# Optimization experiments

Hardware: AMD Instinct MI355X
Metric: run time of the kernel (lower is better)

## Reference

```python
import jax, jax.numpy as jnp
import numpy as np

# dims: batch B, seq S, model D, query heads H, kv heads KV, head_dim HD, group G
B, S, D = 2, 2048, 2048
H, KV, HD = 16, 4, 128
G = H // KV
THETA = 10000.0


def setup_inputs() -> dict:
    key = jax.random.key(0)
    ks = jax.random.split(key, 5)
    x = jax.random.normal(ks[0], (B, S, D), dtype=jnp.float32)
    # RoPE frequencies (real/imag parts of complex freqs_cis)
    inv_freq = 1.0 / (THETA ** (jnp.arange(0, HD, 2, dtype=jnp.float32) / HD))  # (HD/2,)
    t = jnp.arange(S, dtype=jnp.float32)
    freqs = jnp.outer(t, inv_freq)                      # (S, HD/2)
    freqs_cos = jnp.cos(freqs)
    freqs_sin = jnp.sin(freqs)
    # causal additive mask
    mask = jnp.where(jnp.tril(jnp.ones((S, S), dtype=bool)), 0.0, -1e9).astype(jnp.float32)
    sc = 0.02
    wq = jax.random.normal(ks[1], (D, H * HD), dtype=jnp.float32) * sc
    wk = jax.random.normal(ks[2], (D, KV * HD), dtype=jnp.float32) * sc
    wv = jax.random.normal(ks[3], (D, KV * HD), dtype=jnp.float32) * sc
    wo = jax.random.normal(ks[4], (H * HD, D), dtype=jnp.float32) * sc
    return {"x": x, "freqs_cos": freqs_cos, "freqs_sin": freqs_sin, "mask": mask,
            "wq": wq, "wk": wk, "wv": wv, "wo": wo}


def _apply_rope(x, cos, sin):
    # x: (B, S, nh, HD); cos/sin: (S, HD/2). Interleaved complex rotation.
    xr = x.reshape(*x.shape[:-1], HD // 2, 2)
    xe, xo = xr[..., 0], xr[..., 1]
    c = cos[None, :, None, :]
    s = sin[None, :, None, :]
    out_e = xe * c - xo * s
    out_o = xe * s + xo * c
    return jnp.stack([out_e, out_o], axis=-1).reshape(x.shape)


def reference(x, freqs_cos, freqs_sin, mask, wq, wk, wv, wo):
    q = (x @ wq).reshape(B, S, H, HD)
    k = (x @ wk).reshape(B, S, KV, HD)
    v = (x @ wv).reshape(B, S, KV, HD)
    q = _apply_rope(q, freqs_cos, freqs_sin)
    k = _apply_rope(k, freqs_cos, freqs_sin)
    # GQA: group query heads instead of expanding KV (same math as expand)
    qg = q.reshape(B, S, KV, G, HD)
    scale = jnp.sqrt(jnp.float32(HD))
    scores = jnp.einsum('bqkgd,bskd->bkgqs', qg, k) / scale   # (B,KV,G,S,S)
    scores = scores + mask                                     # broadcast (S,S)
    attn = jax.nn.softmax(scores, axis=-1)
    out = jnp.einsum('bkgqs,bskd->bqkgd', attn, v)             # (B,S,KV,G,HD)
    out = out.reshape(B, S, H * HD)
    return out @ wo
```

## Files before the change

kernel.cpp:

```cpp
#include <hip/hip_runtime.h>
#include <type_traits>

typedef short s8v   __attribute__((ext_vector_type(8)));
typedef float f32x4 __attribute__((ext_vector_type(4)));
typedef float f32x16 __attribute__((ext_vector_type(16)));
typedef unsigned int u32x2 __attribute__((ext_vector_type(2)));
typedef unsigned int u32x4 __attribute__((ext_vector_type(4)));

__device__ __forceinline__ unsigned short f2bf(float f) {
    unsigned int u = __builtin_bit_cast(unsigned int, f);
    u += 0x7FFF + ((u >> 16) & 1);
    return (unsigned short)(u >> 16);
}
__device__ __forceinline__ float bf2f(unsigned short b) {
    unsigned int u = ((unsigned int)b) << 16;
    return __builtin_bit_cast(float, u);
}
__device__ __forceinline__ unsigned int cvtpk(float lo, float hi) {
    unsigned int w;
    asm("v_cvt_pk_bf16_f32 %0, %1, %2" : "=v"(w) : "v"(lo), "v"(hi));
    return w;
}

__device__ __forceinline__ void gload16(const void* g, void* l) {
    __builtin_amdgcn_global_load_lds(
        (const __attribute__((address_space(1))) void*)g,
        (__attribute__((address_space(3))) void*)l, 16, 0, 0);
}

__global__ void conv_bf16(const float* __restrict__ src, unsigned short* __restrict__ dst, int n8) {
    int i = blockIdx.x * blockDim.x + threadIdx.x;
    if (i >= n8) return;
    const f32x4* s4 = (const f32x4*)src;
    f32x4 a = s4[2 * i], b = s4[2 * i + 1];
    s8v o;
    o[0] = (short)f2bf(a[0]); o[1] = (short)f2bf(a[1]);
    o[2] = (short)f2bf(a[2]); o[3] = (short)f2bf(a[3]);
    o[4] = (short)f2bf(b[0]); o[5] = (short)f2bf(b[1]);
    o[6] = (short)f2bf(b[2]); o[7] = (short)f2bf(b[3]);
    *(s8v*)(dst + (size_t)i * 8) = o;
}

__global__ void transpose_conv(const float* __restrict__ src, unsigned short* __restrict__ dst,
                               int K, int N) {
    __shared__ float tile[32][33];
    int n0 = blockIdx.x * 32, k0 = blockIdx.y * 32;
    int tx = threadIdx.x, ty = threadIdx.y;
#pragma unroll
    for (int r = 0; r < 4; ++r)
        tile[ty + r * 8][tx] = src[(size_t)(k0 + ty + r * 8) * N + n0 + tx];
    __syncthreads();
#pragma unroll
    for (int r = 0; r < 4; ++r)
        dst[(size_t)(n0 + ty + r * 8) * K + k0 + tx] = f2bf(tile[tx][ty + r * 8]);
}

__global__ void transpose_conv_qkv(const float* __restrict__ wq, const float* __restrict__ wk,
                                   const float* __restrict__ wv, unsigned short* __restrict__ dst) {
    __shared__ float tile[32][33];
    int n0 = blockIdx.x * 32, k0 = blockIdx.y * 32;
    const float* src; int sc, N;
    if (n0 < 2048)      { src = wq; sc = n0;        N = 2048; }
    else if (n0 < 2560) { src = wk; sc = n0 - 2048; N = 512;  }
    else                { src = wv; sc = n0 - 2560; N = 512;  }
    int tx = threadIdx.x, ty = threadIdx.y;
#pragma unroll
    for (int r = 0; r < 4; ++r)
        tile[ty + r * 8][tx] = src[(size_t)(k0 + ty + r * 8) * N + sc + tx];
    __syncthreads();
#pragma unroll
    for (int r = 0; r < 4; ++r)
        dst[(size_t)(n0 + ty + r * 8) * 2048 + k0 + tx] = f2bf(tile[tx][ty + r * 8]);
}

__global__ void vtrans(const unsigned short* __restrict__ qkv, unsigned short* __restrict__ vt) {
    __shared__ unsigned short t[32][33];
    int s0 = blockIdx.x * 32;
    int c0 = blockIdx.y * 32;
    int tx = threadIdx.x, ty = threadIdx.y;
#pragma unroll
    for (int r = 0; r < 4; ++r)
        t[ty + r * 8][tx] = qkv[(size_t)(s0 + ty + r * 8) * 3072 + 2560 + c0 + tx];
    __syncthreads();
    int b = s0 >> 11, s = s0 & 2047;
    size_t dbase = (size_t)(b * 4 + (c0 >> 7)) * 128 + (c0 & 127);
#pragma unroll
    for (int r = 0; r < 4; ++r)
        vt[(dbase + ty + r * 8) * 2048 + s + tx] = t[tx][ty + r * 8];
}

template <typename CT, bool ROPE>
__global__ __launch_bounds__(256)
void gemm_bt(const unsigned short* __restrict__ A, const unsigned short* __restrict__ BT,
             CT* __restrict__ C, const float* __restrict__ fc, const float* __restrict__ fs,
             int M, int N, int K, int ldc) {
    __shared__ unsigned short As[128 * 64];
    __shared__ unsigned short Bs[128 * 64];
    const int tid = threadIdx.x;
    const int wid = tid >> 6, lane = tid & 63;
    const int l31 = lane & 31, h2 = lane >> 5;
    const int nbx = N >> 7;
    const int per = nbx >> 3;
    const int xcd = blockIdx.x & 7;
    const int li  = blockIdx.x >> 3;
    const int bx  = xcd * per + (li % per);
    const int by  = li / per;
    const int brow = by * 128, bcol = bx * 128;
    const int wr = wid >> 1, wc = wid & 1;
    f32x16 acc[2][2] = {};

    for (int kt = 0; kt < K; kt += 64) {
#pragma unroll
        for (int i = 0; i < 4; ++i) {
            int c = i * 256 + tid;
            int row = c >> 3, u = c & 7;
            gload16(A + (size_t)(brow + row) * K + kt + ((u ^ (row & 7)) << 3),
                    As + (size_t)c * 8);
            gload16(BT + (size_t)(bcol + row) * K + kt + ((u ^ (row & 7)) << 3),
                    Bs + (size_t)c * 8);
        }
        __syncthreads();
        s8v a[2][4], b[2][4];
#pragma unroll
        for (int mm = 0; mm < 2; ++mm) {
            int row = wr * 64 + mm * 32 + l31;
#pragma unroll
            for (int ks = 0; ks < 4; ++ks)
                a[mm][ks] = *(const s8v*)(As + (size_t)row * 64 +
                                          (((2 * ks + h2) ^ (row & 7)) << 3));
        }
#pragma unroll
        for (int nn = 0; nn < 2; ++nn) {
            int row = wc * 64 + nn * 32 + l31;
#pragma unroll
            for (int ks = 0; ks < 4; ++ks)
                b[nn][ks] = *(const s8v*)(Bs + (size_t)row * 64 +
                                          (((2 * ks + h2) ^ (row & 7)) << 3));
        }
#pragma unroll
        for (int ks = 0; ks < 4; ++ks)
#pragma unroll
            for (int mm = 0; mm < 2; ++mm)
#pragma unroll
                for (int nn = 0; nn < 2; ++nn)
                    acc[mm][nn] = __builtin_amdgcn_mfma_f32_32x32x16_bf16(
                        a[mm][ks], b[nn][ks], acc[mm][nn], 0, 0, 0);
        __syncthreads();
    }
#pragma unroll
    for (int mm = 0; mm < 2; ++mm)
#pragma unroll
        for (int nn = 0; nn < 2; ++nn)
#pragma unroll
            for (int reg = 0; reg < 16; ++reg) {
                int r = brow + wr * 64 + mm * 32 + (reg & 3) + 8 * (reg >> 2) + 4 * h2;
                int c = bcol + wc * 64 + nn * 32 + l31;
                float v = acc[mm][nn][reg];
                if constexpr (ROPE) {
                    float vp = __shfl_xor(v, 1);
                    if (c < 2560) {
                        int fi = ((r & 2047) << 6) + ((c & 127) >> 1);
                        float cs = fc[fi], sn = fs[fi];
                        v = (l31 & 1) ? (vp * sn + v * cs) : (v * cs - vp * sn);
                    }
                }
                if constexpr (std::is_same<CT, float>::value)
                    C[(size_t)r * ldc + c] = v;
                else
                    C[(size_t)r * ldc + c] = f2bf(v);
            }
}

__global__ __launch_bounds__(256)
void attn_kernel(const unsigned short* __restrict__ qkv,
                 const unsigned short* __restrict__ vtg,
                 unsigned short* __restrict__ out) {
    constexpr int S = 2048;
    __shared__ unsigned short Ks[2][64 * 128];
    __shared__ unsigned short Vs[2][128 * 64];
    const int tid = threadIdx.x, lane = tid & 63, wid = tid >> 6;
    const int l31 = lane & 31, h2 = lane >> 5;
    const int lsw = l31 & 7;
    const int g8 = blockIdx.x & 7;
    const int b = g8 >> 2, kvh = g8 & 3;
    const int qi = 63 - (blockIdx.x >> 3);
    const int h = kvh * 4 + wid;
    const int qw = qi * 32;
    const int qq = qw + l31;
    const size_t rs = 3072;
    const float rscale = 0.08838834764831845f;

    const unsigned short* Qp = qkv + (size_t)(b * S + qw) * rs + h * 128 + h2 * 8;
    const unsigned short* Kbase = qkv + (size_t)(b * S) * rs + 2048 + kvh * 128;
    const unsigned short* Vtg = vtg + (size_t)((b * 4 + kvh) * 128) * S;

    s8v qf[8];
#pragma unroll
    for (int kk = 0; kk < 8; ++kk)
        qf[kk] = *(const s8v*)(Qp + (size_t)l31 * rs + kk * 16);

    f32x16 acc[4] = {};
    float m_run = -1e30f, l_run = 0.f;
    const int nt = (qi >> 1) + 1;

    auto stage = [&](int t, int bufi) {
        const int kb64 = t * 64;
#pragma unroll
        for (int i = 0; i < 4; ++i) {
            int c = i * 256 + tid;
            int key = c >> 4, d8 = c & 15;
            gload16(Kbase + (size_t)(kb64 + key) * rs + ((d8 ^ (key & 7)) << 3),
                    &Ks[bufi][(size_t)c * 8]);
        }
#pragma unroll
        for (int i = 0; i < 4; ++i) {
            int c = i * 256 + tid;
            int d = c >> 3, k8 = c & 7;
            gload16(Vtg + (size_t)d * S + kb64 + ((k8 ^ (d & 7)) << 3),
                    &Vs[bufi][(size_t)c * 8]);
        }
    };

    int cur = 0;
    stage(0, 0);
    __syncthreads();

    for (int t = 0; t < nt; ++t) {
        if (t + 1 < nt) stage(t + 1, cur ^ 1);
        const int kb64 = t * 64;
        const char* Kb = (const char*)&Ks[cur][0];
        const char* Vb = (const char*)&Vs[cur][0];

        s8v kf0[8], kf1[8];
#pragma unroll
        for (int kk = 0; kk < 8; ++kk)
            kf0[kk] = *(const s8v*)(Kb + l31 * 256 + (((2 * kk + h2) ^ lsw) << 4));
#pragma unroll
        for (int kk = 0; kk < 8; ++kk)
            kf1[kk] = *(const s8v*)(Kb + (32 + l31) * 256 + (((2 * kk + h2) ^ lsw) << 4));
        s8v vf[4][4];
#pragma unroll
        for (int kb = 0; kb < 4; ++kb)
#pragma unroll
            for (int dblk = 0; dblk < 4; ++dblk)
                vf[kb][dblk] = *(const s8v*)(Vb + (32 * dblk + l31) * 128 +
                                             (((2 * kb + h2) ^ lsw) << 4));

        f32x16 sacc0 = {}, sacc1 = {};
        __builtin_amdgcn_s_setprio(1);
#pragma unroll
        for (int kk = 0; kk < 8; ++kk)
            sacc0 = __builtin_amdgcn_mfma_f32_32x32x16_bf16(kf0[kk], qf[kk], sacc0, 0, 0, 0);
#pragma unroll
        for (int kk = 0; kk < 8; ++kk)
            sacc1 = __builtin_amdgcn_mfma_f32_32x32x16_bf16(kf1[kk], qf[kk], sacc1, 0, 0, 0);
        __builtin_amdgcn_s_setprio(0);

        float sv[32];
        if (t == nt - 1) {
#pragma unroll
            for (int g = 0; g < 2; ++g)
#pragma unroll
                for (int r = 0; r < 16; ++r) {
                    int key = kb64 + 32 * g + (r & 3) + 8 * (r >> 2) + 4 * h2;
                    float s = (g ? sacc1[r] : sacc0[r]) * rscale;
                    sv[g * 16 + r] = (key <= qq) ? s : -1e30f;
                }
        } else {
#pragma unroll
            for (int r = 0; r < 16; ++r) sv[r] = sacc0[r] * rscale;
#pragma unroll
            for (int r = 0; r < 16; ++r) sv[16 + r] = sacc1[r] * rscale;
        }

        float mx = sv[0];
#pragma unroll
        for (int i = 1; i < 32; ++i) mx = fmaxf(mx, sv[i]);
        mx = fmaxf(mx, __shfl_xor(mx, 32));
        if (!__all(mx - m_run <= 8.f)) {
            float mn = fmaxf(m_run, mx);
            float alpha = __expf(m_run - mn);
            m_run = mn;
            l_run *= alpha;
#pragma unroll
            for (int dblk = 0; dblk < 4; ++dblk)
#pragma unroll
                for (int r = 0; r < 16; ++r) acc[dblk][r] *= alpha;
        }
        float ps = 0.f;
#pragma unroll
        for (int i = 0; i < 32; ++i) {
            float e = __expf(sv[i] - m_run);
            sv[i] = e;
            ps += e;
        }
        ps += __shfl_xor(ps, 32);
        l_run += ps;

        unsigned int pw[4][4];
#pragma unroll
        for (int g = 0; g < 2; ++g) {
            unsigned int w[8];
#pragma unroll
            for (int j = 0; j < 8; ++j)
                w[j] = cvtpk(sv[g * 16 + 2 * j], sv[g * 16 + 2 * j + 1]);
#pragma unroll
            for (int u = 0; u < 2; ++u) {
                unsigned int t0 = (unsigned)__shfl_xor((int)w[4 * u + 0], 32);
                unsigned int t1 = (unsigned)__shfl_xor((int)w[4 * u + 1], 32);
                unsigned int t2 = (unsigned)__shfl_xor((int)w[4 * u + 2], 32);
                unsigned int t3 = (unsigned)__shfl_xor((int)w[4 * u + 3], 32);
                pw[2 * g + u][0] = h2 ? t2 : w[4 * u + 0];
                pw[2 * g + u][1] = h2 ? t3 : w[4 * u + 1];
                pw[2 * g + u][2] = h2 ? w[4 * u + 2] : t0;
                pw[2 * g + u][3] = h2 ? w[4 * u + 3] : t1;
            }
        }

        __builtin_amdgcn_s_setprio(1);
#pragma unroll
        for (int kb = 0; kb < 4; ++kb) {
            u32x4 wv;
            wv[0] = pw[kb][0]; wv[1] = pw[kb][1]; wv[2] = pw[kb][2]; wv[3] = pw[kb][3];
            s8v pf = __builtin_bit_cast(s8v, wv);
#pragma unroll
            for (int dblk = 0; dblk < 4; ++dblk)
                acc[dblk] = __builtin_amdgcn_mfma_f32_32x32x16_bf16(vf[kb][dblk], pf, acc[dblk], 0, 0, 0);
        }
        __builtin_amdgcn_s_setprio(0);

        __syncthreads();
        cur ^= 1;
    }

    float inv = 1.f / l_run;
    unsigned short* Op = out + (size_t)(b * S + qq) * 2048 + h * 128 + 4 * h2;
#pragma unroll
    for (int dblk = 0; dblk < 4; ++dblk)
#pragma unroll
        for (int s = 0; s < 4; ++s) {
            u32x2 wv;
            wv[0] = cvtpk(acc[dblk][4 * s + 0] * inv, acc[dblk][4 * s + 1] * inv);
            wv[1] = cvtpk(acc[dblk][4 * s + 2] * inv, acc[dblk][4 * s + 3] * inv);
            *(u32x2*)(Op + 32 * dblk + 8 * s) = wv;
        }
}

extern "C" void kernel_launch(void* const* d_in, const int* in_sizes, int n_in,
                              void* d_out, int out_size, void* d_ws, size_t ws_size,
                              hipStream_t stream) {
    const float* x  = (const float*)d_in[0];
    const float* fc = (const float*)d_in[1];
    const float* fs = (const float*)d_in[2];
    const float* wq = (const float*)d_in[4];
    const float* wk = (const float*)d_in[5];
    const float* wv = (const float*)d_in[6];
    const float* wo = (const float*)d_in[7];
    float* out = (float*)d_out;

    char* ws = (char*)d_ws;
    unsigned short* xb    = (unsigned short*)ws;
    unsigned short* wqkvT = (unsigned short*)(ws + 16777216);
    unsigned short* woT   = (unsigned short*)(ws + 16777216 + 12582912);
    unsigned short* qkvb  = (unsigned short*)(ws + 16777216 + 12582912 + 8388608);
    unsigned short* attnb = xb;
    unsigned short* vtb   = wqkvT;

    conv_bf16<<<4096, 256, 0, stream>>>(x, xb, 1048576);
    dim3 tb(32, 8);
    transpose_conv_qkv<<<dim3(96, 64), tb, 0, stream>>>(wq, wk, wv, wqkvT);
    transpose_conv<<<dim3(64, 64), tb, 0, stream>>>(wo, woT, 2048, 2048);
    gemm_bt<unsigned short, true><<<768, 256, 0, stream>>>(
        xb, wqkvT, qkvb, fc, fs, 4096, 3072, 2048, 3072);
    vtrans<<<dim3(128, 16), tb, 0, stream>>>(qkvb, vtb);
    attn_kernel<<<512, 256, 0, stream>>>(qkvb, vtb, attnb);
    gemm_bt<float, false><<<512, 256, 0, stream>>>(
        attnb, woT, out, nullptr, nullptr, 4096, 2048, 2048, 2048);
}
```

Before: 231.8 us.

## Double-buffer GEMM shared tiles and fold attention scale into Q projection

The GEMM now stages the next K-tile of A and B into a second shared-memory buffer while computing on the current one, and raises wave priority around the MFMA block. This hides global load latency behind compute instead of serializing load, sync and compute. The softmax scale is also applied to Q columns in the QKV GEMM epilogue, which removes per-score multiplies in the attention kernel. Shared memory per block doubles, which may reduce occupancy, and scaling before the bf16 rounding slightly changes numerics.

```diff
diff --git a/kernel.cpp b/kernel.cpp
--- a/kernel.cpp
+++ b/kernel.cpp
@@ -94,8 +94,8 @@
 void gemm_bt(const unsigned short* __restrict__ A, const unsigned short* __restrict__ BT,
              CT* __restrict__ C, const float* __restrict__ fc, const float* __restrict__ fs,
              int M, int N, int K, int ldc) {
-    __shared__ unsigned short As[128 * 64];
-    __shared__ unsigned short Bs[128 * 64];
+    __shared__ unsigned short As[2][128 * 64];
+    __shared__ unsigned short Bs[2][128 * 64];
     const int tid = threadIdx.x;
     const int wid = tid >> 6, lane = tid & 63;
     const int l31 = lane & 31, h2 = lane >> 5;
@@ -109,24 +109,33 @@
     const int wr = wid >> 1, wc = wid & 1;
     f32x16 acc[2][2] = {};
 
-    for (int kt = 0; kt < K; kt += 64) {
+    auto stage = [&](int kt, int bufi) {
 #pragma unroll
         for (int i = 0; i < 4; ++i) {
             int c = i * 256 + tid;
             int row = c >> 3, u = c & 7;
             gload16(A + (size_t)(brow + row) * K + kt + ((u ^ (row & 7)) << 3),
-                    As + (size_t)c * 8);
+                    &As[bufi][(size_t)c * 8]);
             gload16(BT + (size_t)(bcol + row) * K + kt + ((u ^ (row & 7)) << 3),
-                    Bs + (size_t)c * 8);
-        }
-        __syncthreads();
+                    &Bs[bufi][(size_t)c * 8]);
+        }
+    };
+
+    int cur = 0;
+    stage(0, 0);
+    __syncthreads();
+
+    for (int kt = 0; kt < K; kt += 64) {
+        if (kt + 64 < K) stage(kt + 64, cur ^ 1);
+        const unsigned short* Ab = &As[cur][0];
+        const unsigned short* Bb = &Bs[cur][0];
         s8v a[2][4], b[2][4];
 #pragma unroll
         for (int mm = 0; mm < 2; ++mm) {
             int row = wr * 64 + mm * 32 + l31;
 #pragma unroll
             for (int ks = 0; ks < 4; ++ks)
-                a[mm][ks] = *(const s8v*)(As + (size_t)row * 64 +
+                a[mm][ks] = *(const s8v*)(Ab + (size_t)row * 64 +
                                           (((2 * ks + h2) ^ (row & 7)) << 3));
         }
 #pragma unroll
@@ -134,9 +143,10 @@
             int row = wc * 64 + nn * 32 + l31;
 #pragma unroll
             for (int ks = 0; ks < 4; ++ks)
-                b[nn][ks] = *(const s8v*)(Bs + (size_t)row * 64 +
+                b[nn][ks] = *(const s8v*)(Bb + (size_t)row * 64 +
                                           (((2 * ks + h2) ^ (row & 7)) << 3));
         }
+        __builtin_amdgcn_s_setprio(1);
 #pragma unroll
         for (int ks = 0; ks < 4; ++ks)
 #pragma unroll
@@ -145,7 +155,9 @@
                 for (int nn = 0; nn < 2; ++nn)
                     acc[mm][nn] = __builtin_amdgcn_mfma_f32_32x32x16_bf16(
                         a[mm][ks], b[nn][ks], acc[mm][nn], 0, 0, 0);
+        __builtin_amdgcn_s_setprio(0);
         __syncthreads();
+        cur ^= 1;
     }
 #pragma unroll
     for (int mm = 0; mm < 2; ++mm)
@@ -163,6 +175,7 @@
                         float cs = fc[fi], sn = fs[fi];
                         v = (l31 & 1) ? (vp * sn + v * cs) : (v * cs - vp * sn);
                     }
+                    if (c < 2048) v *= 0.08838834764831845f;
                 }
                 if constexpr (std::is_same<CT, float>::value)
                     C[(size_t)r * ldc + c] = v;
@@ -188,7 +201,6 @@
     const int qw = qi * 32;
     const int qq = qw + l31;
     const size_t rs = 3072;
-    const float rscale = 0.08838834764831845f;
 
     const unsigned short* Qp = qkv + (size_t)(b * S + qw) * rs + h * 128 + h2 * 8;
     const unsigned short* Kbase = qkv + (size_t)(b * S) * rs + 2048 + kvh * 128;
@@ -263,14 +275,14 @@
 #pragma unroll
                 for (int r = 0; r < 16; ++r) {
                     int key = kb64 + 32 * g + (r & 3) + 8 * (r >> 2) + 4 * h2;
-                    float s = (g ? sacc1[r] : sacc0[r]) * rscale;
+                    float s = (g ? sacc1[r] : sacc0[r]);
                     sv[g * 16 + r] = (key <= qq) ? s : -1e30f;
                 }
         } else {
 #pragma unroll
-            for (int r = 0; r < 16; ++r) sv[r] = sacc0[r] * rscale;
-#pragma unroll
-            for (int r = 0; r < 16; ++r) sv[16 + r] = sacc1[r] * rscale;
+            for (int r = 0; r < 16; ++r) sv[r] = sacc0[r];
+#pragma unroll
+            for (int r = 0; r < 16; ++r) sv[16 + r] = sacc1[r];
         }
 
         float mx = sv[0];
```

Result: slower. 269.4 us (+16.2%).
